# Optimization experiments

Hardware: AMD Instinct MI355X
Metric: run time of the kernel (lower is better)

The kernel has to match this reference:

```python
import jax, jax.numpy as jnp
import numpy as np

NUM_TYPES = 4
IN_DIM = 128
HID_DIM = 256
OUT_DIM = 128
NUM_NODES = 100000


def setup_inputs() -> dict:
    key = jax.random.key(0)
    k_x, k_t, k_w1, k_b1, k_w2, k_b2 = jax.random.split(key, 6)
    raw_features = jax.random.normal(k_x, (NUM_NODES, IN_DIM), dtype=jnp.float32)
    node_type = jax.random.randint(k_t, (NUM_NODES,), 0, NUM_TYPES, dtype=jnp.int64)
    # stacked per-type MLP params (Kaiming-ish scale like torch Linear defaults)
    W1 = jax.random.uniform(k_w1, (NUM_TYPES, IN_DIM, HID_DIM), dtype=jnp.float32,
                            minval=-1.0, maxval=1.0) / np.sqrt(IN_DIM)
    b1 = jax.random.uniform(k_b1, (NUM_TYPES, HID_DIM), dtype=jnp.float32,
                            minval=-1.0, maxval=1.0) / np.sqrt(IN_DIM)
    W2 = jax.random.uniform(k_w2, (NUM_TYPES, HID_DIM, OUT_DIM), dtype=jnp.float32,
                            minval=-1.0, maxval=1.0) / np.sqrt(HID_DIM)
    b2 = jax.random.uniform(k_b2, (NUM_TYPES, OUT_DIM), dtype=jnp.float32,
                            minval=-1.0, maxval=1.0) / np.sqrt(HID_DIM)
    return {"raw_features": raw_features, "node_type": node_type,
            "W1": W1, "b1": b1, "W2": W2, "b2": b2}


def reference(raw_features, node_type, W1, b1, W2, b2):
    # Run every expert on every node (num_types is tiny), then select per node.
    # h: [types, nodes, hidden]
    h = jax.nn.relu(jnp.einsum('ni,tih->tnh', raw_features, W1) + b1[:, None, :])
    # out_all: [types, nodes, out]
    out_all = jnp.einsum('tnh,tho->tno', h, W2) + b2[:, None, :]
    # select expert output matching each node's type -> [nodes, out]
    encoded = out_all[node_type, jnp.arange(raw_features.shape[0])]
    return encoded
```

## Files before the change

### kernel.cpp

```cpp
#include <hip/hip_runtime.h>

typedef float f32x4 __attribute__((ext_vector_type(4)));
typedef short short8 __attribute__((ext_vector_type(8)));

#define NTYPES 4


static __device__ __forceinline__ unsigned short f2bf(float f) {
  union { float f; unsigned int u; } v; v.f = f;
  unsigned int u = v.u;
  unsigned int r = u + 0x7FFFu + ((u >> 16) & 1u);
  return (unsigned short)(r >> 16);
}

#define LGKM_BAR() do { \
  asm volatile("s_waitcnt lgkmcnt(0)" ::: "memory"); \
  __builtin_amdgcn_s_barrier(); \
  __builtin_amdgcn_sched_barrier(0); } while (0)

__global__ __launch_bounds__(256) void k_prep(const float* __restrict__ W1,
                                              const float* __restrict__ W2,
                                              unsigned short* __restrict__ W1T,
                                              unsigned short* __restrict__ W2T,
                                              int* __restrict__ meta) {
  __shared__ unsigned short s[64][72];
  const int tid = threadIdx.x;
  const int b = blockIdx.x;
  if (b == 0 && tid < 16) meta[tid] = 0;
  const int bb = b & 31;
  const int t = bb >> 3, ti = bb & 7;
  const float* src; unsigned short* dst; int scols, tr, tc;
  if (b < 32) { src = W1 + t * 32768; dst = W1T + t * 32768; scols = 256; tr = ti >> 2; tc = ti & 3; }
  else        { src = W2 + t * 32768; dst = W2T + t * 32768; scols = 128; tr = ti >> 1; tc = ti & 1; }
  const int srows = 32768 / scols;
  const int r0 = tid >> 4, c4 = (tid & 15) << 2;
  #pragma unroll
  for (int i = 0; i < 4; ++i) {
    int r = tr * 64 + i * 16 + r0;
    float4 v = *(const float4*)(src + r * scols + tc * 64 + c4);
    s[i * 16 + r0][c4 + 0] = f2bf(v.x);
    s[i * 16 + r0][c4 + 1] = f2bf(v.y);
    s[i * 16 + r0][c4 + 2] = f2bf(v.z);
    s[i * 16 + r0][c4 + 3] = f2bf(v.w);
  }
  __syncthreads();
  #pragma unroll
  for (int i = 0; i < 4; ++i) {
    int orow = i * 16 + r0;
    ushort4 u;
    u.x = s[c4 + 0][orow];
    u.y = s[c4 + 1][orow];
    u.z = s[c4 + 2][orow];
    u.w = s[c4 + 3][orow];
    *(ushort4*)(dst + (tc * 64 + orow) * srows + tr * 64 + c4) = u;
  }
}

__global__ __launch_bounds__(256) void k_hist(const int* __restrict__ NT, int n,
                                              int* __restrict__ meta) {
  __shared__ int c[NTYPES];
  if (threadIdx.x < NTYPES) c[threadIdx.x] = 0;
  __syncthreads();
  int i = blockIdx.x * 256 + threadIdx.x;
  if (i < n) atomicAdd(&c[NT[i]], 1);
  __syncthreads();
  if (threadIdx.x < NTYPES && c[threadIdx.x] > 0)
    atomicAdd(&meta[threadIdx.x], c[threadIdx.x]);
}

__global__ __launch_bounds__(256) void k_scatter(const int* __restrict__ NT, int n,
                                                 int* __restrict__ meta,
                                                 int* __restrict__ perm) {
  __shared__ int cnt[NTYPES];
  __shared__ int cbase[NTYPES];
  __shared__ int sb[NTYPES + 1];
  if (threadIdx.x < NTYPES) cnt[threadIdx.x] = 0;
  if (threadIdx.x == 0) {
    int b = 0; sb[0] = 0;
    for (int t = 0; t < NTYPES; ++t) {
      b += (meta[t] + 63) & ~63;
      sb[t + 1] = b;
    }
  }
  __syncthreads();
  int i = blockIdx.x * 256 + threadIdx.x;
  int t = 0, r = 0;
  bool valid = (i < n);
  if (valid) { t = NT[i]; r = atomicAdd(&cnt[t], 1); }
  __syncthreads();
  if (threadIdx.x < NTYPES)
    cbase[threadIdx.x] = atomicAdd(&meta[4 + threadIdx.x], cnt[threadIdx.x]);
  __syncthreads();
  if (valid) perm[sb[t] + cbase[t] + r] = i;
  if (blockIdx.x == 0) {
    if (threadIdx.x <= NTYPES) meta[8 + threadIdx.x] = sb[threadIdx.x];
    int tt = threadIdx.x >> 6, j = threadIdx.x & 63;
    int p = sb[tt] + meta[tt] + j;
    if (p < sb[tt + 1]) perm[p] = -1;
  }
}

__global__ __launch_bounds__(512, 2) void k_mlpw(
    const float* __restrict__ X, const int* __restrict__ perm,
    const int* __restrict__ meta,
    const unsigned short* __restrict__ W1T, const unsigned short* __restrict__ W2T,
    const float* __restrict__ B1, const float* __restrict__ B2,
    float* __restrict__ OUT, float* __restrict__ dump) {
  __shared__ __align__(16) unsigned char x_lds[16384];
  __shared__ __align__(16) unsigned char h_lds[32768];

  const int tid = threadIdx.x;
  const int l  = tid & 63, w = tid >> 6;
  const int lo = l & 15,  hi = l >> 4;

  const int t  = blockIdx.x >> 7;
  const int lb = blockIdx.x & 127;
  const int g0 = meta[8 + t] >> 6;
  const int g1 = meta[9 + t] >> 6;
  const int nt = g1 - g0 - lb;
  if (nt <= 0) return;
  const int cnt = (nt + 127) >> 7;

  const int gr = tid >> 3;
  const int gq = tid & 7;

  int pm = perm[(g0 + lb) * 64 + gr];
  float4 xv0 = make_float4(0.f, 0.f, 0.f, 0.f), xv1 = xv0, xv2 = xv0, xv3 = xv0;
  if (pm >= 0) {
    const float4* s = (const float4*)(X + (size_t)pm * 128 + gq * 16);
    xv0 = s[0]; xv1 = s[1]; xv2 = s[2]; xv3 = s[3];
  }

  const unsigned short* w1t = W1T + (t << 15);
  const unsigned short* w2t = W2T + (t << 15);
  short8 a1[4][2], a2[8];
  #pragma unroll
  for (int ks = 0; ks < 4; ++ks)
    #pragma unroll
    for (int m = 0; m < 2; ++m)
      a1[ks][m] = *(const short8*)(w1t + (w * 32 + m * 16 + lo) * 128 + ks * 32 + hi * 8);
  #pragma unroll
  for (int ks = 0; ks < 8; ++ks)
    a2[ks] = *(const short8*)(w2t + (w * 16 + lo) * 256 + ks * 32 + hi * 8);
  f32x4 bb1[2], bb2;
  #pragma unroll
  for (int m = 0; m < 2; ++m)
    bb1[m] = *(const f32x4*)(B1 + t * 256 + w * 32 + m * 16 + hi * 4);
  bb2 = *(const f32x4*)(B2 + t * 128 + w * 16 + hi * 4);

  for (int j = 0; j < cnt; ++j) {
    const int g = g0 + lb + j * 128;
    const bool hn = (j + 1 < cnt);

    {
      short8 c0, c1;
      c0[0] = (short)f2bf(xv0.x); c0[1] = (short)f2bf(xv0.y);
      c0[2] = (short)f2bf(xv0.z); c0[3] = (short)f2bf(xv0.w);
      c0[4] = (short)f2bf(xv1.x); c0[5] = (short)f2bf(xv1.y);
      c0[6] = (short)f2bf(xv1.z); c0[7] = (short)f2bf(xv1.w);
      c1[0] = (short)f2bf(xv2.x); c1[1] = (short)f2bf(xv2.y);
      c1[2] = (short)f2bf(xv2.z); c1[3] = (short)f2bf(xv2.w);
      c1[4] = (short)f2bf(xv3.x); c1[5] = (short)f2bf(xv3.y);
      c1[6] = (short)f2bf(xv3.z); c1[7] = (short)f2bf(xv3.w);
      const int base = gr * 256 + gq * 32;
      const int swz = (gr & 7) << 4;
      *(short8*)(x_lds + (base ^ swz)) = c0;
      *(short8*)(x_lds + ((base + 16) ^ swz)) = c1;
    }
    LGKM_BAR();

    int pm2 = -1;
    if (hn) pm2 = perm[(g + 128) * 64 + gr];

    f32x4 acc[2][4];
    #pragma unroll
    for (int m = 0; m < 2; ++m)
      #pragma unroll
      for (int n = 0; n < 4; ++n) acc[m][n] = (f32x4){0.f, 0.f, 0.f, 0.f};
    #pragma unroll
    for (int ks = 0; ks < 4; ++ks) {
      const int k8 = ks * 32 + hi * 8;
      short8 b[4];
      #pragma unroll
      for (int n = 0; n < 4; ++n) {
        int row = n * 16 + lo;
        int byte = (row * 256 + k8 * 2) ^ ((row & 7) << 4);
        b[n] = *(const short8*)(x_lds + byte);
      }
      #pragma unroll
      for (int m = 0; m < 2; ++m)
        #pragma unroll
        for (int n = 0; n < 4; ++n)
          acc[m][n] = __builtin_amdgcn_mfma_f32_16x16x32_bf16(a1[ks][m], b[n], acc[m][n], 0, 0, 0);
    }

    #pragma unroll
    for (int m = 0; m < 2; ++m) {
      const int hc = w * 32 + m * 16 + hi * 4;
      #pragma unroll
      for (int n = 0; n < 4; ++n) {
        int row = n * 16 + lo;
        ushort4 hv;
        hv.x = f2bf(fmaxf(acc[m][n][0] + bb1[m][0], 0.f));
        hv.y = f2bf(fmaxf(acc[m][n][1] + bb1[m][1], 0.f));
        hv.z = f2bf(fmaxf(acc[m][n][2] + bb1[m][2], 0.f));
        hv.w = f2bf(fmaxf(acc[m][n][3] + bb1[m][3], 0.f));
        int byte = (row * 512 + hc * 2) ^ ((row & 7) << 4);
        *(ushort4*)(h_lds + byte) = hv;
      }
    }
    LGKM_BAR();

    f32x4 acc2[4];
    #pragma unroll
    for (int n = 0; n < 4; ++n) acc2[n] = (f32x4){0.f, 0.f, 0.f, 0.f};
    #pragma unroll
    for (int ks = 0; ks < 8; ++ks) {
      const int k8 = ks * 32 + hi * 8;
      short8 b[4];
      #pragma unroll
      for (int n = 0; n < 4; ++n) {
        int row = n * 16 + lo;
        int byte = (row * 512 + k8 * 2) ^ ((row & 7) << 4);
        b[n] = *(const short8*)(h_lds + byte);
      }
      #pragma unroll
      for (int n = 0; n < 4; ++n)
        acc2[n] = __builtin_amdgcn_mfma_f32_16x16x32_bf16(a2[ks], b[n], acc2[n], 0, 0, 0);
    }

    int rid[4];
    #pragma unroll
    for (int p = 0; p < 4; ++p) rid[p] = perm[g * 64 + p * 16 + (tid >> 5)];

    LGKM_BAR();

    #pragma unroll
    for (int n = 0; n < 4; ++n) {
      int row = n * 16 + lo;
      const int oc = w * 16 + hi * 4;
      f32x4 o = acc2[n];
      o[0] += bb2[0]; o[1] += bb2[1]; o[2] += bb2[2]; o[3] += bb2[3];
      int byte = (row * 512 + oc * 4) ^ ((row & 7) << 4);
      *(f32x4*)(h_lds + byte) = o;
    }

    float4 nv0 = make_float4(0.f, 0.f, 0.f, 0.f), nv1 = nv0, nv2 = nv0, nv3 = nv0;
    if (pm2 >= 0) {
      const float4* s = (const float4*)(X + (size_t)pm2 * 128 + gq * 16);
      nv0 = s[0]; nv1 = s[1]; nv2 = s[2]; nv3 = s[3];
    }

    LGKM_BAR();

    #pragma unroll
    for (int p = 0; p < 4; ++p) {
      int off = p * 8192 + tid * 16;
      int row = off >> 9;
      f32x4 v = *(const f32x4*)(h_lds + (off ^ ((row & 7) << 4)));
      int colf = (off & 511) >> 2;
      float* dst = (rid[p] >= 0) ? (OUT + (size_t)rid[p] * 128 + colf) : (dump + colf);
      *(f32x4*)dst = v;
    }

    xv0 = nv0; xv1 = nv1; xv2 = nv2; xv3 = nv3;
  }
}

extern "C" void kernel_launch(void* const* d_in, const int* in_sizes, int n_in,
                              void* d_out, int out_size, void* d_ws, size_t ws_size,
                              hipStream_t stream) {
  const float* X  = (const float*)d_in[0];
  const int*   NT = (const int*)d_in[1];
  const float* W1 = (const float*)d_in[2];
  const float* B1 = (const float*)d_in[3];
  const float* W2 = (const float*)d_in[4];
  const float* B2 = (const float*)d_in[5];
  float* OUT = (float*)d_out;
  const int n = in_sizes[1];

  char* ws = (char*)d_ws;
  int* meta = (int*)ws;
  float* dump = (float*)(ws + 512);
  int* perm = (int*)(ws + 1024);
  unsigned short* W1T = (unsigned short*)(ws + 402432);
  unsigned short* W2T = (unsigned short*)(ws + 664576);

  k_prep<<<64, 256, 0, stream>>>(W1, W2, W1T, W2T, meta);
  const int nb = (n + 255) / 256;
  k_hist<<<nb, 256, 0, stream>>>(NT, n, meta);
  k_scatter<<<nb, 256, 0, stream>>>(NT, n, meta, perm);
  k_mlpw<<<512, 512, 0, stream>>>(X, perm, meta, W1T, W2T, B1, B2, OUT, dump);
}
```

Baseline: 59.59 us.

## Halve MLP block to 4 waves with larger per-wave tiles and direct output stores

```diff
diff --git a/kernel.cpp b/kernel.cpp
--- a/kernel.cpp
+++ b/kernel.cpp
@@ -100,7 +100,7 @@
   }
 }
 
-__global__ __launch_bounds__(512, 2) void k_mlpw(
+__global__ __launch_bounds__(256, 2) void k_mlpw(
     const float* __restrict__ X, const int* __restrict__ perm,
     const int* __restrict__ meta,
     const unsigned short* __restrict__ W1T, const unsigned short* __restrict__ W2T,
@@ -121,149 +121,151 @@
   if (nt <= 0) return;
   const int cnt = (nt + 127) >> 7;
 
-  const int gr = tid >> 3;
-  const int gq = tid & 7;
+  const int gr = tid >> 2;
+  const int gq = tid & 3;
 
   int pm = perm[(g0 + lb) * 64 + gr];
-  float4 xv0 = make_float4(0.f, 0.f, 0.f, 0.f), xv1 = xv0, xv2 = xv0, xv3 = xv0;
+  float4 xv[8];
+  #pragma unroll
+  for (int i = 0; i < 8; ++i) xv[i] = make_float4(0.f, 0.f, 0.f, 0.f);
   if (pm >= 0) {
-    const float4* s = (const float4*)(X + (size_t)pm * 128 + gq * 16);
-    xv0 = s[0]; xv1 = s[1]; xv2 = s[2]; xv3 = s[3];
+    const float4* s = (const float4*)(X + (size_t)pm * 128 + gq * 32);
+    #pragma unroll
+    for (int i = 0; i < 8; ++i) xv[i] = s[i];
   }
 
   const unsigned short* w1t = W1T + (t << 15);
   const unsigned short* w2t = W2T + (t << 15);
-  short8 a1[4][2], a2[8];
+  short8 a1[4][4];
   #pragma unroll
   for (int ks = 0; ks < 4; ++ks)
     #pragma unroll
-    for (int m = 0; m < 2; ++m)
-      a1[ks][m] = *(const short8*)(w1t + (w * 32 + m * 16 + lo) * 128 + ks * 32 + hi * 8);
+    for (int m = 0; m < 4; ++m)
+      a1[ks][m] = *(const short8*)(w1t + (w * 64 + m * 16 + lo) * 128 + ks * 32 + hi * 8);
+  short8 a2[8][2];
   #pragma unroll
   for (int ks = 0; ks < 8; ++ks)
-    a2[ks] = *(const short8*)(w2t + (w * 16 + lo) * 256 + ks * 32 + hi * 8);
-  f32x4 bb1[2], bb2;
-  #pragma unroll
-  for (int m = 0; m < 2; ++m)
-    bb1[m] = *(const f32x4*)(B1 + t * 256 + w * 32 + m * 16 + hi * 4);
-  bb2 = *(const f32x4*)(B2 + t * 128 + w * 16 + hi * 4);
+    #pragma unroll
+    for (int mo = 0; mo < 2; ++mo)
+      a2[ks][mo] = *(const short8*)(w2t + (w * 32 + mo * 16 + lo) * 256 + ks * 32 + hi * 8);
+  f32x4 bb1[4], bb2[2];
+  #pragma unroll
+  for (int m = 0; m < 4; ++m)
+    bb1[m] = *(const f32x4*)(B1 + t * 256 + w * 64 + m * 16 + hi * 4);
+  #pragma unroll
+  for (int mo = 0; mo < 2; ++mo)
+    bb2[mo] = *(const f32x4*)(B2 + t * 128 + w * 32 + mo * 16 + hi * 4);
 
   for (int j = 0; j < cnt; ++j) {
     const int g = g0 + lb + j * 128;
     const bool hn = (j + 1 < cnt);
 
     {
-      short8 c0, c1;
-      c0[0] = (short)f2bf(xv0.x); c0[1] = (short)f2bf(xv0.y);
-      c0[2] = (short)f2bf(xv0.z); c0[3] = (short)f2bf(xv0.w);
-      c0[4] = (short)f2bf(xv1.x); c0[5] = (short)f2bf(xv1.y);
-      c0[6] = (short)f2bf(xv1.z); c0[7] = (short)f2bf(xv1.w);
-      c1[0] = (short)f2bf(xv2.x); c1[1] = (short)f2bf(xv2.y);
-      c1[2] = (short)f2bf(xv2.z); c1[3] = (short)f2bf(xv2.w);
-      c1[4] = (short)f2bf(xv3.x); c1[5] = (short)f2bf(xv3.y);
-      c1[6] = (short)f2bf(xv3.z); c1[7] = (short)f2bf(xv3.w);
-      const int base = gr * 256 + gq * 32;
+      const int rbase = gr * 256;
       const int swz = (gr & 7) << 4;
-      *(short8*)(x_lds + (base ^ swz)) = c0;
-      *(short8*)(x_lds + ((base + 16) ^ swz)) = c1;
+      #pragma unroll
+      for (int q = 0; q < 4; ++q) {
+        short8 c;
+        float4 va = xv[2 * q], vb = xv[2 * q + 1];
+        c[0] = (short)f2bf(va.x); c[1] = (short)f2bf(va.y);
+        c[2] = (short)f2bf(va.z); c[3] = (short)f2bf(va.w);
+        c[4] = (short)f2bf(vb.x); c[5] = (short)f2bf(vb.y);
+        c[6] = (short)f2bf(vb.z); c[7] = (short)f2bf(vb.w);
+        int byte = (rbase + gq * 64 + q * 16) ^ swz;
+        *(short8*)(x_lds + byte) = c;
+      }
     }
     LGKM_BAR();
 
-    int pm2 = -1;
-    if (hn) pm2 = perm[(g + 128) * 64 + gr];
-
-    f32x4 acc[2][4];
-    #pragma unroll
-    for (int m = 0; m < 2; ++m)
+    int pmn = -1;
+    if (hn) pmn = perm[(g + 128) * 64 + gr];
+    int rid[4];
+    #pragma unroll
+    for (int n = 0; n < 4; ++n) rid[n] = perm[g * 64 + n * 16 + lo];
+
+    f32x4 acc[4][4];
+    #pragma unroll
+    for (int m = 0; m < 4; ++m)
       #pragma unroll
       for (int n = 0; n < 4; ++n) acc[m][n] = (f32x4){0.f, 0.f, 0.f, 0.f};
     #pragma unroll
     for (int ks = 0; ks < 4; ++ks) {
-      const int k8 = ks * 32 + hi * 8;
       short8 b[4];
       #pragma unroll
       for (int n = 0; n < 4; ++n) {
         int row = n * 16 + lo;
-        int byte = (row * 256 + k8 * 2) ^ ((row & 7) << 4);
+        int byte = (row * 256 + ks * 64 + hi * 16) ^ ((row & 7) << 4);
         b[n] = *(const short8*)(x_lds + byte);
       }
       #pragma unroll
-      for (int m = 0; m < 2; ++m)
+      for (int m = 0; m < 4; ++m)
         #pragma unroll
         for (int n = 0; n < 4; ++n)
           acc[m][n] = __builtin_amdgcn_mfma_f32_16x16x32_bf16(a1[ks][m], b[n], acc[m][n], 0, 0, 0);
     }
 
     #pragma unroll
-    for (int m = 0; m < 2; ++m) {
-      const int hc = w * 32 + m * 16 + hi * 4;
-      #pragma unroll
-      for (int n = 0; n < 4; ++n) {
-        int row = n * 16 + lo;
+    for (int m = 0; m < 4; ++m) {
+      const int hw2 = w * 128 + m * 32 + hi * 8;
+      #pragma unroll
+      for (int n = 0; n < 4; ++n) {
+        int node = n * 16 + lo;
         ushort4 hv;
         hv.x = f2bf(fmaxf(acc[m][n][0] + bb1[m][0], 0.f));
         hv.y = f2bf(fmaxf(acc[m][n][1] + bb1[m][1], 0.f));
         hv.z = f2bf(fmaxf(acc[m][n][2] + bb1[m][2], 0.f));
         hv.w = f2bf(fmaxf(acc[m][n][3] + bb1[m][3], 0.f));
-        int byte = (row * 512 + hc * 2) ^ ((row & 7) << 4);
+        int byte = (node * 512 + hw2) ^ ((node & 7) << 4);
         *(ushort4*)(h_lds + byte) = hv;
       }
     }
     LGKM_BAR();
 
-    f32x4 acc2[4];
-    #pragma unroll
-    for (int n = 0; n < 4; ++n) acc2[n] = (f32x4){0.f, 0.f, 0.f, 0.f};
+    float4 nv[8];
+    #pragma unroll
+    for (int i = 0; i < 8; ++i) nv[i] = make_float4(0.f, 0.f, 0.f, 0.f);
+    if (pmn >= 0) {
+      const float4* s = (const float4*)(X + (size_t)pmn * 128 + gq * 32);
+      #pragma unroll
+      for (int i = 0; i < 8; ++i) nv[i] = s[i];
+    }
+
+    f32x4 acc2[2][4];
+    #pragma unroll
+    for (int mo = 0; mo < 2; ++mo)
+      #pragma unroll
+      for (int n = 0; n < 4; ++n) acc2[mo][n] = (f32x4){0.f, 0.f, 0.f, 0.f};
     #pragma unroll
     for (int ks = 0; ks < 8; ++ks) {
-      const int k8 = ks * 32 + hi * 8;
       short8 b[4];
       #pragma unroll
       for (int n = 0; n < 4; ++n) {
-        int row = n * 16 + lo;
-        int byte = (row * 512 + k8 * 2) ^ ((row & 7) << 4);
+        int node = n * 16 + lo;
+        int byte = (node * 512 + ks * 64 + hi * 16) ^ ((node & 7) << 4);
         b[n] = *(const short8*)(h_lds + byte);
       }
       #pragma unroll
-      for (int n = 0; n < 4; ++n)
-        acc2[n] = __builtin_amdgcn_mfma_f32_16x16x32_bf16(a2[ks], b[n], acc2[n], 0, 0, 0);
-    }
-
-    int rid[4];
-    #pragma unroll
-    for (int p = 0; p < 4; ++p) rid[p] = perm[g * 64 + p * 16 + (tid >> 5)];
-
-    LGKM_BAR();
-
-    #pragma unroll
-    for (int n = 0; n < 4; ++n) {
-      int row = n * 16 + lo;
-      const int oc = w * 16 + hi * 4;
-      f32x4 o = acc2[n];
-      o[0] += bb2[0]; o[1] += bb2[1]; o[2] += bb2[2]; o[3] += bb2[3];
-      int byte = (row * 512 + oc * 4) ^ ((row & 7) << 4);
-      *(f32x4*)(h_lds + byte) = o;
-    }
-
-    float4 nv0 = make_float4(0.f, 0.f, 0.f, 0.f), nv1 = nv0, nv2 = nv0, nv3 = nv0;
-    if (pm2 >= 0) {
-      const float4* s = (const float4*)(X + (size_t)pm2 * 128 + gq * 16);
-      nv0 = s[0]; nv1 = s[1]; nv2 = s[2]; nv3 = s[3];
-    }
-
-    LGKM_BAR();
-
-    #pragma unroll
-    for (int p = 0; p < 4; ++p) {
-      int off = p * 8192 + tid * 16;
-      int row = off >> 9;
-      f32x4 v = *(const f32x4*)(h_lds + (off ^ ((row & 7) << 4)));
-      int colf = (off & 511) >> 2;
-      float* dst = (rid[p] >= 0) ? (OUT + (size_t)rid[p] * 128 + colf) : (dump + colf);
-      *(f32x4*)dst = v;
-    }
-
-    xv0 = nv0; xv1 = nv1; xv2 = nv2; xv3 = nv3;
+      for (int mo = 0; mo < 2; ++mo)
+        #pragma unroll
+        for (int n = 0; n < 4; ++n)
+          acc2[mo][n] = __builtin_amdgcn_mfma_f32_16x16x32_bf16(a2[ks][mo], b[n], acc2[mo][n], 0, 0, 0);
+    }
+
+    #pragma unroll
+    for (int mo = 0; mo < 2; ++mo) {
+      const int oc = w * 32 + mo * 16 + hi * 4;
+      #pragma unroll
+      for (int n = 0; n < 4; ++n) {
+        f32x4 o = acc2[mo][n];
+        o[0] += bb2[mo][0]; o[1] += bb2[mo][1];
+        o[2] += bb2[mo][2]; o[3] += bb2[mo][3];
+        float* dst = (rid[n] >= 0) ? (OUT + (size_t)rid[n] * 128 + oc) : (dump + oc);
+        *(f32x4*)dst = o;
+      }
+    }
+
+    #pragma unroll
+    for (int i = 0; i < 8; ++i) xv[i] = nv[i];
   }
 }
 
@@ -290,5 +292,5 @@
   const int nb = (n + 255) / 256;
   k_hist<<<nb, 256, 0, stream>>>(NT, n, meta);
   k_scatter<<<nb, 256, 0, stream>>>(NT, n, meta, perm);
-  k_mlpw<<<512, 512, 0, stream>>>(X, perm, meta, W1T, W2T, B1, B2, OUT, dump);
-}
+  k_mlpw<<<512, 256, 0, stream>>>(X, perm, meta, W1T, W2T, B1, B2, OUT, dump);
+}
```

After: 118.5 us. +98.9%, slower.
